# Performance work log

Hardware: AMD Instinct MI355X
Metric: run time of the kernel (lower is better)

## Reference

```python
import jax, jax.numpy as jnp
import numpy as np

D_MODEL, D_FF, D_NEURON, D_HIDDEN = 512, 2048, 128, 256
PHI_IN = D_NEURON + 1  # 129
EPS = 1e-5


def _ln(x, g, b):
    mu = x.mean(-1, keepdims=True)
    var = ((x - mu) ** 2).mean(-1, keepdims=True)
    return (x - mu) * jax.lax.rsqrt(var + EPS) * g + b


def _gelu(x):
    return jax.nn.gelu(x, approximate=False)


def setup_inputs() -> dict:
    key = jax.random.key(0)
    ks = jax.random.split(key, 16)
    s = 0.02
    inp = {
        'x': jax.random.normal(ks[0], (4, 1024, D_MODEL), jnp.float32),
        'W_in': jax.random.normal(ks[1], (D_FF, D_MODEL), jnp.float32) * s,
        'neuron_vecs': jax.random.normal(ks[2], (D_FF, D_NEURON), jnp.float32) * s,
        'Wr1': jax.random.normal(ks[3], (D_MODEL, D_MODEL), jnp.float32) * s,
        'Wr2': jax.random.normal(ks[4], (D_FF, D_MODEL), jnp.float32) * s,
        'rn_g': jnp.ones((D_MODEL,), jnp.float32),
        'rn_b': jnp.zeros((D_MODEL,), jnp.float32),
        'pW1': jax.random.normal(ks[5], (PHI_IN, D_HIDDEN), jnp.float32) * (1.0 / np.sqrt(PHI_IN)),
        'pb1': jnp.zeros((D_HIDDEN,), jnp.float32),
        'pln1_g': jnp.ones((D_HIDDEN,), jnp.float32),
        'pln1_b': jnp.zeros((D_HIDDEN,), jnp.float32),
        'pW2': jax.random.normal(ks[6], (D_HIDDEN, D_HIDDEN), jnp.float32) * (1.0 / np.sqrt(D_HIDDEN)),
        'pb2': jnp.zeros((D_HIDDEN,), jnp.float32),
        'pln2_g': jnp.ones((D_HIDDEN,), jnp.float32),
        'pln2_b': jnp.zeros((D_HIDDEN,), jnp.float32),
        'rln_g': jnp.ones((D_HIDDEN,), jnp.float32),
        'rln_b': jnp.zeros((D_HIDDEN,), jnp.float32),
        'rW1': jax.random.normal(ks[7], (D_HIDDEN, 2 * D_HIDDEN), jnp.float32) * (1.0 / np.sqrt(D_HIDDEN)),
        'rb1': jnp.zeros((2 * D_HIDDEN,), jnp.float32),
        'rW2': jax.random.normal(ks[8], (2 * D_HIDDEN, D_MODEL), jnp.float32) * (1.0 / np.sqrt(2 * D_HIDDEN)),
        'rb2': jnp.zeros((D_MODEL,), jnp.float32),
        'top_k': 64,
    }
    return inp


def reference(x, W_in, neuron_vecs, Wr1, Wr2, rn_g, rn_b,
              pW1, pb1, pln1_g, pln1_b, pW2, pb2, pln2_g, pln2_b,
              rln_g, rln_b, rW1, rb1, rW2, rb2, top_k):
    batch, seq, d_model = x.shape
    xf = x.reshape(-1, d_model)  # [T, D]

    # Router (MLP variant): LN -> GELU(x @ Wr1^T) -> @ Wr2^T
    h = _gelu(_ln(xf, rn_g, rn_b) @ Wr1.T)
    scores = h @ Wr2.T  # [T, d_ff]
    _, idx = jax.lax.top_k(scores, top_k)  # [T, K]

    # Gather selected neuron params (irregular access)
    W_sel = W_in[idx]           # [T, K, D]
    nv_sel = neuron_vecs[idx]   # [T, K, d_neuron]

    # Per-token activations for selected neurons
    act = _gelu(jnp.einsum('td,tkd->tk', xf, W_sel))  # [T, K]

    # phi: Linear -> LN -> GELU -> Linear -> LN
    phi_in = jnp.concatenate([nv_sel, act[..., None]], axis=-1)  # [T, K, 129]
    hphi = _ln(phi_in @ pW1 + pb1, pln1_g, pln1_b)
    hphi = _gelu(hphi)
    hphi = _ln(hphi @ pW2 + pb2, pln2_g, pln2_b)  # [T, K, d_hidden]

    agg = hphi.sum(axis=1)  # [T, d_hidden]

    # rho: LN -> Linear -> GELU -> (Dropout eval=identity) -> Linear
    r = _ln(agg, rln_g, rln_b)
    r = _gelu(r @ rW1 + rb1)
    out = r @ rW2 + rb2  # [T, d_model]
    return out.reshape(batch, seq, d_model)
```

## Files before the change

kernel.cpp:

```cpp
#include <hip/hip_runtime.h>
#include <cstdint>
#include <cstddef>

typedef unsigned short u16;
typedef float f32x4 __attribute__((ext_vector_type(4)));
typedef short short8 __attribute__((ext_vector_type(8)));
typedef int i32x4 __attribute__((ext_vector_type(4)));


__device__ __forceinline__ float geluf(float v) {
  return 0.5f * v * (1.0f + erff(v * 0.70710678118654752440f));
}

__device__ __forceinline__ float erf_fast(float x) {
  const float ax = fabsf(x);
  const float t = __builtin_amdgcn_rcpf(fmaf(0.3275911f, ax, 1.0f));
  float p = fmaf(1.061405429f, t, -1.453152027f);
  p = fmaf(p, t, 1.421413741f);
  p = fmaf(p, t, -0.284496736f);
  p = fmaf(p, t, 0.254829592f);
  p = p * t;
  const float e = __expf(-ax * ax);
  const float r = fmaf(-p, e, 1.0f);
  return copysignf(r, x);
}
__device__ __forceinline__ float gelu_fast(float v) {
  return 0.5f * v * (1.0f + erf_fast(v * 0.70710678118654752440f));
}

__device__ __forceinline__ u16 f2bf(float f) {
  unsigned u = __float_as_uint(f);
  u = (u + 0x7FFFu + ((u >> 16) & 1u)) >> 16;
  return (u16)u;
}
__device__ __forceinline__ float bf2f(u16 h) {
  return __uint_as_float(((unsigned)h) << 16);
}

__device__ __forceinline__ void waveRed2(float& s, float& s2) {
#pragma unroll
  for (int m = 1; m < 64; m <<= 1) {
    s += __shfl_xor(s, m);
    s2 += __shfl_xor(s2, m);
  }
}

__global__ __launch_bounds__(256) void k_ln512(const float* __restrict__ x,
                                               const float* __restrict__ g,
                                               const float* __restrict__ b,
                                               float* __restrict__ out) {
  __shared__ float red[8];
  const int t = blockIdx.x, tid = threadIdx.x;
  const float v0 = x[(size_t)t * 512 + tid];
  const float v1 = x[(size_t)t * 512 + 256 + tid];
  float s = v0 + v1, s2 = v0 * v0 + v1 * v1;
  waveRed2(s, s2);
  if ((tid & 63) == 0) { red[(tid >> 6) * 2] = s; red[(tid >> 6) * 2 + 1] = s2; }
  __syncthreads();
  s = red[0] + red[2] + red[4] + red[6];
  s2 = red[1] + red[3] + red[5] + red[7];
  const float mu = s * (1.f / 512.f);
  const float var = fmaxf(s2 * (1.f / 512.f) - mu * mu, 0.f);
  const float rstd = 1.f / sqrtf(var + 1e-5f);
  out[(size_t)t * 512 + tid] = (v0 - mu) * rstd * g[tid] + b[tid];
  out[(size_t)t * 512 + 256 + tid] = (v1 - mu) * rstd * g[tid + 256] + b[tid + 256];
}

__global__ __launch_bounds__(256) void k_cvt(const float* __restrict__ in,
                                             u16* __restrict__ o) {
  const int i = blockIdx.x * 256 + threadIdx.x;
  o[i] = f2bf(in[i]);
}

__global__ __launch_bounds__(256) void k_splitT(const float* __restrict__ in,
                                                u16* __restrict__ hiT,
                                                u16* __restrict__ loT, int R,
                                                int Cc) {
  const int n = blockIdx.x;
  for (int k = threadIdx.x; k < R; k += 256) {
    const float v = in[(size_t)k * Cc + n];
    const u16 h = f2bf(v);
    hiT[(size_t)n * R + k] = h;
    loT[(size_t)n * R + k] = f2bf(v - bf2f(h));
  }
}

__global__ __launch_bounds__(256) void k_nvphi(const float* __restrict__ nv,
                                               const float* __restrict__ pW1,
                                               const float* __restrict__ pb1,
                                               float* __restrict__ nvphi) {
  __shared__ float nvs[128];
  const int n = blockIdx.x, tid = threadIdx.x;
  if (tid < 128) nvs[tid] = nv[n * 128 + tid];
  __syncthreads();
  float s = pb1[tid];
#pragma unroll 4
  for (int i = 0; i < 128; ++i) s = fmaf(nvs[i], pW1[i * 256 + tid], s);
  nvphi[n * 256 + tid] = s;
}

__global__ __launch_bounds__(256) void k_pw2t(const float* __restrict__ pW2,
                                              u16* __restrict__ pW2T) {
  const int n = blockIdx.x, k = threadIdx.x;
  pW2T[n * 256 + k] = f2bf(pW2[k * 256 + n]);
}

template <int GMODE, bool BF16OUT>
__global__ __launch_bounds__(256) void gemm_bt(const float* __restrict__ A,
                                               const float* __restrict__ B,
                                               float* __restrict__ C,
                                               u16* __restrict__ Cb, int M,
                                               int N, int K) {
  __shared__ float As[16][68];
  __shared__ float Bs[16][68];
  const int tid = threadIdx.x;
  const int tn = tid & 15, tm = tid >> 4;
  const int m0 = blockIdx.y * 64, n0 = blockIdx.x * 64;
  const int lr = tid >> 2, lk = (tid & 3) << 2;
  float acc[4][4] = {};
  for (int k0 = 0; k0 < K; k0 += 16) {
    const float4 av = *(const float4*)&A[(size_t)(m0 + lr) * K + k0 + lk];
    const float4 bv = *(const float4*)&B[(size_t)(n0 + lr) * K + k0 + lk];
    As[lk + 0][lr] = av.x; As[lk + 1][lr] = av.y; As[lk + 2][lr] = av.z; As[lk + 3][lr] = av.w;
    Bs[lk + 0][lr] = bv.x; Bs[lk + 1][lr] = bv.y; Bs[lk + 2][lr] = bv.z; Bs[lk + 3][lr] = bv.w;
    __syncthreads();
#pragma unroll
    for (int k = 0; k < 16; ++k) {
      float a[4], b[4];
      *(float4*)a = *(const float4*)&As[k][tm * 4];
      *(float4*)b = *(const float4*)&Bs[k][tn * 4];
#pragma unroll
      for (int i = 0; i < 4; ++i)
#pragma unroll
        for (int j = 0; j < 4; ++j) acc[i][j] = fmaf(a[i], b[j], acc[i][j]);
    }
    __syncthreads();
  }
#pragma unroll
  for (int i = 0; i < 4; ++i) {
    float4 v;
    float* vp = (float*)&v;
#pragma unroll
    for (int j = 0; j < 4; ++j) {
      float xv = acc[i][j];
      if (GMODE == 2) xv = geluf(xv);
      vp[j] = xv;
    }
    const size_t off = (size_t)(m0 + tm * 4 + i) * N + n0 + tn * 4;
    *(float4*)&C[off] = v;
    if (BF16OUT) {
      ushort4 ob;
      ob.x = f2bf(vp[0]); ob.y = f2bf(vp[1]); ob.z = f2bf(vp[2]); ob.w = f2bf(vp[3]);
      *(ushort4*)&Cb[off] = ob;
    }
  }
}

template <bool SPLIT, int GMODE, bool BIAS, int OUT>
__global__ __launch_bounds__(256) void gemm_mf(
    const u16* __restrict__ Ahi, const u16* __restrict__ Alo,
    const u16* __restrict__ Bhi, const u16* __restrict__ Blo,
    const float* __restrict__ bias, void* __restrict__ Cp,
    void* __restrict__ C2p, int M, int N, int K) {
  constexpr int ASZ = 64 * 40;
  constexpr int BSZ = 128 * 40;
  __shared__ __align__(16) u16 smem[(SPLIT ? 2 : 1) * (ASZ + BSZ)];
  u16* sAh = smem;
  u16* sBh = smem + (SPLIT ? 2 : 1) * ASZ;
  u16* sAl = SPLIT ? (smem + ASZ) : nullptr;
  u16* sBl = SPLIT ? (sBh + BSZ) : nullptr;

  const int tid = threadIdx.x;
  const int w = tid >> 6, lane = tid & 63;
  const int q = lane >> 4, c = lane & 15;
  const int m0 = blockIdx.y * 64, n0 = blockIdx.x * 128;
  const int ra = tid >> 2, ka = (tid & 3) * 8;
  const int rb = tid >> 1, kb = (tid & 1) * 16;
  const u16* gAh = Ahi + (size_t)(m0 + ra) * K + ka;
  const u16* gBh = Bhi + (size_t)(n0 + rb) * K + kb;
  const u16* gAl = SPLIT ? (Alo + (size_t)(m0 + ra) * K + ka) : nullptr;
  const u16* gBl = SPLIT ? (Blo + (size_t)(n0 + rb) * K + kb) : nullptr;

  f32x4 acc[8];
#pragma unroll
  for (int ct = 0; ct < 8; ++ct) {
    const float bv = BIAS ? bias[n0 + ct * 16 + c] : 0.f;
    acc[ct] = (f32x4){bv, bv, bv, bv};
  }

  for (int k0 = 0; k0 < K; k0 += 32) {
    const i32x4 vah = *(const i32x4*)(gAh + k0);
    const i32x4 vbh0 = *(const i32x4*)(gBh + k0);
    const i32x4 vbh1 = *(const i32x4*)(gBh + k0 + 8);
    i32x4 val, vbl0, vbl1;
    if (SPLIT) {
      val = *(const i32x4*)(gAl + k0);
      vbl0 = *(const i32x4*)(gBl + k0);
      vbl1 = *(const i32x4*)(gBl + k0 + 8);
    }
    __syncthreads();
    *(i32x4*)&sAh[ra * 40 + ka] = vah;
    *(i32x4*)&sBh[rb * 40 + kb] = vbh0;
    *(i32x4*)&sBh[rb * 40 + kb + 8] = vbh1;
    if (SPLIT) {
      *(i32x4*)&sAl[ra * 40 + ka] = val;
      *(i32x4*)&sBl[rb * 40 + kb] = vbl0;
      *(i32x4*)&sBl[rb * 40 + kb + 8] = vbl1;
    }
    __syncthreads();
    const int abase = (w * 16 + c) * 40 + q * 8;
    const short8 ah = *(const short8*)&sAh[abase];
    short8 al;
    if (SPLIT) al = *(const short8*)&sAl[abase];
#pragma unroll
    for (int ct = 0; ct < 8; ++ct) {
      const int bbase = (ct * 16 + c) * 40 + q * 8;
      const short8 bh = *(const short8*)&sBh[bbase];
      acc[ct] = __builtin_amdgcn_mfma_f32_16x16x32_bf16(ah, bh, acc[ct], 0, 0, 0);
      if (SPLIT) {
        const short8 bl = *(const short8*)&sBl[bbase];
        acc[ct] = __builtin_amdgcn_mfma_f32_16x16x32_bf16(al, bh, acc[ct], 0, 0, 0);
        acc[ct] = __builtin_amdgcn_mfma_f32_16x16x32_bf16(ah, bl, acc[ct], 0, 0, 0);
      }
    }
  }
#pragma unroll
  for (int ct = 0; ct < 8; ++ct) {
#pragma unroll
    for (int reg = 0; reg < 4; ++reg) {
      float v = acc[ct][reg];
      if (GMODE == 1) v = gelu_fast(v);
      const size_t off = (size_t)(m0 + w * 16 + q * 4 + reg) * N + n0 + ct * 16 + c;
      if (OUT == 0) {
        ((float*)Cp)[off] = v;
      } else if (OUT == 1) {
        ((u16*)Cp)[off] = f2bf(v);
      } else {
        const u16 hv = f2bf(v);
        ((u16*)Cp)[off] = hv;
        ((u16*)C2p)[off] = f2bf(v - bf2f(hv));
      }
    }
  }
}

__global__ __launch_bounds__(256) void k_topk_rs(
    const u16* __restrict__ scoresb, const float* __restrict__ h,
    const float* __restrict__ Wr2, int* __restrict__ idxout) {
  __shared__ float hs[512];
  __shared__ int redc[4];
  __shared__ int cand[160];
  __shared__ float cex[160];
  __shared__ unsigned ccnt, cg_cnt, ec;
  __shared__ int eqbuf[64];
  const int t = blockIdx.x, tid = threadIdx.x;
  hs[tid] = h[(size_t)t * 512 + tid];
  hs[tid + 256] = h[(size_t)t * 512 + 256 + tid];
  unsigned key[8];
#pragma unroll
  for (int j = 0; j < 8; ++j) {
    const unsigned u = ((unsigned)scoresb[(size_t)t * 2048 + tid + 256 * j]) << 16;
    key[j] = (u & 0x80000000u) ? ~u : (u | 0x80000000u);
  }
  if (tid == 0) ccnt = 0u;
  unsigned lo = 0u, hi = 0xFFFFFFFFu;
  while (lo < hi) {
    const unsigned mid = (unsigned)(((unsigned long long)lo + hi + 1ull) >> 1);
    int c = 0;
#pragma unroll
    for (int j = 0; j < 8; ++j) c += (key[j] >= mid);
#pragma unroll
    for (int m = 1; m < 64; m <<= 1) c += __shfl_xor(c, m);
    if ((tid & 63) == 0) redc[tid >> 6] = c;
    __syncthreads();
    const int total = redc[0] + redc[1] + redc[2] + redc[3];
    __syncthreads();
    if (total >= 96) lo = mid; else hi = mid - 1;
  }
#pragma unroll
  for (int j = 0; j < 8; ++j) {
    if (key[j] >= lo) {
      const unsigned pos = atomicAdd(&ccnt, 1u);
      if (pos < 160u) cand[pos] = tid + 256 * j;
    }
  }
  __syncthreads();
  const int cnt = (int)(ccnt < 160u ? ccnt : 160u);
  const int wv = tid >> 6, l = tid & 63;
  for (int ci = wv; ci < cnt; ci += 4) {
    const float* Wr = Wr2 + (size_t)cand[ci] * 512;
    float s = 0.f;
#pragma unroll
    for (int j = 0; j < 8; ++j) s = fmaf(Wr[l + 64 * j], hs[l + 64 * j], s);
#pragma unroll
    for (int m = 1; m < 64; m <<= 1) s += __shfl_xor(s, m);
    if (l == 0) cex[ci] = s;
  }
  __syncthreads();
  unsigned k2 = 0u;
  int myidx = -1;
  const bool valid = tid < cnt;
  if (valid) {
    const unsigned u = __float_as_uint(cex[tid]);
    k2 = (u & 0x80000000u) ? ~u : (u | 0x80000000u);
    myidx = cand[tid];
  }
  if (tid == 0) { cg_cnt = 0u; ec = 0u; }
  lo = 0u; hi = 0xFFFFFFFFu;
  while (lo < hi) {
    const unsigned mid = (unsigned)(((unsigned long long)lo + hi + 1ull) >> 1);
    int c = (valid && k2 >= mid) ? 1 : 0;
#pragma unroll
    for (int m = 1; m < 64; m <<= 1) c += __shfl_xor(c, m);
    if ((tid & 63) == 0) redc[tid >> 6] = c;
    __syncthreads();
    const int total = redc[0] + redc[1] + redc[2] + redc[3];
    __syncthreads();
    if (total >= 64) lo = mid; else hi = mid - 1;
  }
  if (valid && k2 > lo) {
    const unsigned pos = atomicAdd(&cg_cnt, 1u);
    idxout[(size_t)t * 64 + pos] = myidx;
  } else if (valid && k2 == lo) {
    const unsigned e = atomicAdd(&ec, 1u);
    if (e < 64u) eqbuf[e] = myidx;
  }
  __syncthreads();
  if (tid == 0) {
    const int cg = (int)cg_cnt;
    int ne = (int)ec; if (ne > 64) ne = 64;
    const int need = 64 - cg;
    for (int i = 1; i < ne; ++i) {
      const int v = eqbuf[i];
      int j = i - 1;
      while (j >= 0 && eqbuf[j] > v) { eqbuf[j + 1] = eqbuf[j]; --j; }
      eqbuf[j + 1] = v;
    }
    for (int i = 0; i < need; ++i) idxout[(size_t)t * 64 + cg + i] = eqbuf[i];
  }
}

__global__ __launch_bounds__(256) void k_act(const float* __restrict__ x,
                                             const float* __restrict__ W_in,
                                             const int* __restrict__ idx,
                                             float* __restrict__ act) {
  __shared__ float xs[512];
  const int t = blockIdx.x, tid = threadIdx.x;
  xs[tid] = x[(size_t)t * 512 + tid];
  xs[tid + 256] = x[(size_t)t * 512 + 256 + tid];
  __syncthreads();
  const int w = tid >> 6, l = tid & 63;
  for (int q = 0; q < 16; ++q) {
    const int k = w * 16 + q;
    const int n = idx[(size_t)t * 64 + k];
    const float* Wr = W_in + (size_t)n * 512;
    float s = 0.f;
#pragma unroll
    for (int j = 0; j < 8; ++j) s = fmaf(Wr[l + 64 * j], xs[l + 64 * j], s);
#pragma unroll
    for (int m = 1; m < 64; m <<= 1) s += __shfl_xor(s, m);
    if (l == 0) act[(size_t)t * 64 + k] = gelu_fast(s);
  }
}

__global__ __launch_bounds__(256, 1) void k_phi(
    const float* __restrict__ nvphi, const float* __restrict__ pW1,
    const float* __restrict__ pln1_g, const float* __restrict__ pln1_b,
    const u16* __restrict__ pW2T, const float* __restrict__ pb2,
    const float* __restrict__ pln2_g, const float* __restrict__ pln2_b,
    const int* __restrict__ idx, const float* __restrict__ act,
    float* __restrict__ aggp) {
  __shared__ __align__(16) u16 h1s[64 * 264];
  __shared__ __align__(16) u16 Bs[64 * 264];
  __shared__ float aggbuf[4 * 256];
  __shared__ int idxs[64];
  __shared__ float acts[64];
  const int tid = threadIdx.x;
  const int t = blockIdx.x;
  const int w = tid >> 6, lane = tid & 63;
  const int q = lane >> 4, c = lane & 15;
  if (tid < 64) {
    idxs[tid] = idx[(size_t)t * 64 + tid];
    acts[tid] = act[(size_t)t * 64 + tid];
  }
  __syncthreads();
  {
    f32x4 w4[4], g1[4], b1[4];
#pragma unroll
    for (int j = 0; j < 4; ++j) {
      w4[j] = *(const f32x4*)&pW1[128 * 256 + c * 16 + j * 4];
      g1[j] = *(const f32x4*)&pln1_g[c * 16 + j * 4];
      b1[j] = *(const f32x4*)&pln1_b[c * 16 + j * 4];
    }
#pragma unroll 1
    for (int rd = 0; rd < 4; ++rd) {
      const int p = w * 16 + rd * 4 + q;
      const int n = idxs[p];
      const float av = acts[p];
      f32x4 v[4];
      float s = 0.f, s2 = 0.f;
#pragma unroll
      for (int j = 0; j < 4; ++j) {
        const f32x4 nv = *(const f32x4*)&nvphi[(size_t)n * 256 + c * 16 + j * 4];
#pragma unroll
        for (int u = 0; u < 4; ++u) {
          v[j][u] = nv[u] + av * w4[j][u];
          s += v[j][u];
          s2 = fmaf(v[j][u], v[j][u], s2);
        }
      }
#pragma unroll
      for (int m = 1; m < 16; m <<= 1) { s += __shfl_xor(s, m); s2 += __shfl_xor(s2, m); }
      const float mu = s * (1.f / 256.f);
      const float var = fmaxf(s2 * (1.f / 256.f) - mu * mu, 0.f);
      const float rstd = 1.f / sqrtf(var + 1e-5f);
      short8 lo, hi;
#pragma unroll
      for (int j = 0; j < 4; ++j)
#pragma unroll
        for (int u = 0; u < 4; ++u) {
          const float hv = gelu_fast((v[j][u] - mu) * rstd * g1[j][u] + b1[j][u]);
          if (j < 2) lo[j * 4 + u] = (short)f2bf(hv);
          else       hi[(j - 2) * 4 + u] = (short)f2bf(hv);
        }
      *(short8*)&h1s[p * 264 + c * 16] = lo;
      *(short8*)&h1s[p * 264 + c * 16 + 8] = hi;
    }
  }
  __syncthreads();
  short8 afr[8];
#pragma unroll
  for (int ks = 0; ks < 8; ++ks)
    afr[ks] = *(const short8*)&h1s[(w * 16 + c) * 264 + ks * 32 + q * 8];
  f32x4 acc[16];
#pragma unroll
  for (int nt = 0; nt < 16; ++nt) {
    const float bz = pb2[nt * 16 + c];
    acc[nt] = (f32x4){bz, bz, bz, bz};
  }
#pragma unroll
  for (int ch = 0; ch < 4; ++ch) {
    __syncthreads();
#pragma unroll
    for (int i = 0; i < 8; ++i) {
      const int cidx = i * 256 + tid;
      const int n = cidx >> 5, kc = cidx & 31;
      *(i32x4*)&Bs[n * 264 + kc * 8] =
          *(const i32x4*)&pW2T[(size_t)(ch * 64 + n) * 256 + kc * 8];
    }
    __syncthreads();
#pragma unroll
    for (int t4 = 0; t4 < 4; ++t4) {
      const int nt = ch * 4 + t4;
#pragma unroll
      for (int ks = 0; ks < 8; ++ks) {
        const short8 bfr = *(const short8*)&Bs[(t4 * 16 + c) * 264 + ks * 32 + q * 8];
        acc[nt] = __builtin_amdgcn_mfma_f32_16x16x32_bf16(afr[ks], bfr, acc[nt], 0, 0, 0);
      }
    }
  }
  float g2v[16], b2v[16];
#pragma unroll
  for (int nt = 0; nt < 16; ++nt) {
    g2v[nt] = pln2_g[nt * 16 + c];
    b2v[nt] = pln2_b[nt * 16 + c];
  }
  float aggl[16];
#pragma unroll
  for (int nt = 0; nt < 16; ++nt) aggl[nt] = 0.f;
#pragma unroll
  for (int reg = 0; reg < 4; ++reg) {
    float s = 0.f, s2 = 0.f;
#pragma unroll
    for (int nt = 0; nt < 16; ++nt) {
      const float vv = acc[nt][reg];
      s += vv;
      s2 = fmaf(vv, vv, s2);
    }
#pragma unroll
    for (int m = 1; m < 16; m <<= 1) { s += __shfl_xor(s, m); s2 += __shfl_xor(s2, m); }
    const float mu = s * (1.f / 256.f);
    const float var = fmaxf(s2 * (1.f / 256.f) - mu * mu, 0.f);
    const float rstd = 1.f / sqrtf(var + 1e-5f);
#pragma unroll
    for (int nt = 0; nt < 16; ++nt) {
      const float vv = acc[nt][reg];
      aggl[nt] += (vv - mu) * rstd * g2v[nt] + b2v[nt];
    }
  }
#pragma unroll
  for (int nt = 0; nt < 16; ++nt) {
    float vs = aggl[nt];
    vs += __shfl_xor(vs, 16);
    vs += __shfl_xor(vs, 32);
    if (q == 0) aggbuf[w * 256 + nt * 16 + c] = vs;
  }
  __syncthreads();
  aggp[(size_t)t * 256 + tid] =
      aggbuf[tid] + aggbuf[256 + tid] + aggbuf[512 + tid] + aggbuf[768 + tid];
}

__global__ __launch_bounds__(256) void k_rln(const float* __restrict__ aggp,
                                             const float* __restrict__ g,
                                             const float* __restrict__ b,
                                             u16* __restrict__ rh,
                                             u16* __restrict__ rl) {
  __shared__ float red[8];
  const int t = blockIdx.x, tid = threadIdx.x;
  const float v = aggp[(size_t)t * 256 + tid];
  float s = v, s2 = v * v;
  waveRed2(s, s2);
  if ((tid & 63) == 0) { red[(tid >> 6) * 2] = s; red[(tid >> 6) * 2 + 1] = s2; }
  __syncthreads();
  s = red[0] + red[2] + red[4] + red[6];
  s2 = red[1] + red[3] + red[5] + red[7];
  const float mu = s * (1.f / 256.f);
  const float var = fmaxf(s2 * (1.f / 256.f) - mu * mu, 0.f);
  const float rstd = 1.f / sqrtf(var + 1e-5f);
  const float y = (v - mu) * rstd * g[tid] + b[tid];
  const u16 hv = f2bf(y);
  rh[(size_t)t * 256 + tid] = hv;
  rl[(size_t)t * 256 + tid] = f2bf(y - bf2f(hv));
}

extern "C" void kernel_launch(void* const* d_in, const int* in_sizes, int n_in,
                              void* d_out, int out_size, void* d_ws, size_t ws_size,
                              hipStream_t stream) {
  const float* x = (const float*)d_in[0];
  const float* W_in = (const float*)d_in[1];
  const float* nv = (const float*)d_in[2];
  const float* Wr1 = (const float*)d_in[3];
  const float* Wr2 = (const float*)d_in[4];
  const float* rn_g = (const float*)d_in[5];
  const float* rn_b = (const float*)d_in[6];
  const float* pW1 = (const float*)d_in[7];
  const float* pb1 = (const float*)d_in[8];
  const float* pln1_g = (const float*)d_in[9];
  const float* pln1_b = (const float*)d_in[10];
  const float* pW2 = (const float*)d_in[11];
  const float* pb2 = (const float*)d_in[12];
  const float* pln2_g = (const float*)d_in[13];
  const float* pln2_b = (const float*)d_in[14];
  const float* rln_g = (const float*)d_in[15];
  const float* rln_b = (const float*)d_in[16];
  const float* rW1 = (const float*)d_in[17];
  const float* rb1 = (const float*)d_in[18];
  const float* rW2 = (const float*)d_in[19];
  const float* rb2 = (const float*)d_in[20];
  float* out = (float*)d_out;
  const int T = in_sizes[0] / 512;

  float* ws = (float*)d_ws;
  float* xln = ws;    ws += (size_t)T * 512;
  float* h = ws;      ws += (size_t)T * 512;
  float* nvphi = ws;  ws += (size_t)2048 * 256;
  float* actb = ws;   ws += (size_t)T * 64;
  float* aggp = ws;   ws += (size_t)T * 256;
  int* idx = (int*)ws;   ws += (size_t)T * 64;
  u16* scoresb = (u16*)ws; ws += (size_t)T * 2048 / 2;
  u16* hb = (u16*)ws;    ws += (size_t)T * 512 / 2;
  u16* Wr2b = (u16*)ws;  ws += (size_t)2048 * 512 / 2;
  u16* pW2T = (u16*)ws;  ws += (size_t)2048 * 256 / 2;
  u16* rh = (u16*)ws;    ws += (size_t)T * 256 / 2;
  u16* rl = (u16*)ws;    ws += (size_t)T * 256 / 2;
  u16* t1h = (u16*)ws;   ws += (size_t)T * 512 / 2;
  u16* t1l = (u16*)ws;   ws += (size_t)T * 512 / 2;
  u16* rW1Th = (u16*)ws; ws += (size_t)512 * 256 / 2;
  u16* rW1Tl = (u16*)ws; ws += (size_t)512 * 256 / 2;
  u16* rW2Th = (u16*)ws; ws += (size_t)512 * 512 / 2;
  u16* rW2Tl = (u16*)ws; ws += (size_t)512 * 512 / 2;

  k_cvt<<<2048 * 512 / 256, 256, 0, stream>>>(Wr2, Wr2b);
  k_splitT<<<512, 256, 0, stream>>>(rW1, rW1Th, rW1Tl, 256, 512);
  k_splitT<<<512, 256, 0, stream>>>(rW2, rW2Th, rW2Tl, 512, 512);
  k_nvphi<<<2048, 256, 0, stream>>>(nv, pW1, pb1, nvphi);
  k_pw2t<<<256, 256, 0, stream>>>(pW2, pW2T);
  k_ln512<<<T, 256, 0, stream>>>(x, rn_g, rn_b, xln);
  gemm_bt<2, true><<<dim3(512 / 64, T / 64), 256, 0, stream>>>(
      xln, Wr1, h, hb, T, 512, 512);
  gemm_mf<false, 0, false, 1><<<dim3(2048 / 128, T / 64), 256, 0, stream>>>(
      hb, nullptr, Wr2b, nullptr, nullptr, scoresb, nullptr, T, 2048, 512);
  k_topk_rs<<<T, 256, 0, stream>>>(scoresb, h, Wr2, idx);
  k_act<<<T, 256, 0, stream>>>(x, W_in, idx, actb);
  k_phi<<<T, 256, 0, stream>>>(nvphi, pW1, pln1_g, pln1_b, pW2T, pb2, pln2_g,
                               pln2_b, idx, actb, aggp);
  k_rln<<<T, 256, 0, stream>>>(aggp, rln_g, rln_b, rh, rl);
  gemm_mf<true, 1, true, 2><<<dim3(512 / 128, T / 64), 256, 0, stream>>>(
      rh, rl, rW1Th, rW1Tl, rb1, t1h, t1l, T, 512, 256);
  gemm_mf<true, 0, true, 0><<<dim3(512 / 128, T / 64), 256, 0, stream>>>(
      t1h, t1l, rW2Th, rW2Tl, rb2, out, nullptr, T, 512, 512);
}
```

Measured before the change: 500.7 us.

## Drop split-bf16 in rho GEMMs, retile router GEMM, vectorize act, shrink phi smem

The rho-stage GEMMs now use a single bf16 pass in place of the hi/lo split (three MFMAs per step become one), which removes the lo buffers and their conversions. The router's first fp32 GEMM moves from 64x64 tiles with 4x4 per thread to 128x128 tiles with 8x8 per thread. Top-k's first radix search now runs over 16-bit keys, k_act uses float4 loads, and k_phi halves its B staging buffer and reuses h1s for aggregation to raise occupancy. The change trades accuracy in the rho MLP for less work, and the larger GEMM tiles launch far fewer blocks.

```diff
diff --git a/kernel.cpp b/kernel.cpp
--- a/kernel.cpp
+++ b/kernel.cpp
@@ -72,17 +72,12 @@
   o[i] = f2bf(in[i]);
 }
 
-__global__ __launch_bounds__(256) void k_splitT(const float* __restrict__ in,
-                                                u16* __restrict__ hiT,
-                                                u16* __restrict__ loT, int R,
-                                                int Cc) {
+__global__ __launch_bounds__(256) void k_cvtT(const float* __restrict__ in,
+                                              u16* __restrict__ outT, int R,
+                                              int Cc) {
   const int n = blockIdx.x;
-  for (int k = threadIdx.x; k < R; k += 256) {
-    const float v = in[(size_t)k * Cc + n];
-    const u16 h = f2bf(v);
-    hiT[(size_t)n * R + k] = h;
-    loT[(size_t)n * R + k] = f2bf(v - bf2f(h));
-  }
+  for (int k = threadIdx.x; k < R; k += 256)
+    outT[(size_t)n * R + k] = f2bf(in[(size_t)k * Cc + n]);
 }
 
 __global__ __launch_bounds__(256) void k_nvphi(const float* __restrict__ nv,
@@ -106,69 +101,80 @@
 }
 
 template <int GMODE, bool BF16OUT>
-__global__ __launch_bounds__(256) void gemm_bt(const float* __restrict__ A,
-                                               const float* __restrict__ B,
-                                               float* __restrict__ C,
-                                               u16* __restrict__ Cb, int M,
+__global__ __launch_bounds__(256) void gemm8f(const float* __restrict__ A,
+                                              const float* __restrict__ B,
+                                              float* __restrict__ C,
+                                              u16* __restrict__ Cb, int M,
+                                              int N, int K) {
+  __shared__ float As[16][132];
+  __shared__ float Bs[16][132];
+  const int tid = threadIdx.x;
+  const int tm = tid >> 4, tn = tid & 15;
+  const int m0 = blockIdx.y * 128, n0 = blockIdx.x * 128;
+  const int sr = tid >> 1, sk = (tid & 1) * 8;
+  const float* gA = &A[(size_t)(m0 + sr) * K + sk];
+  const float* gB = &B[(size_t)(n0 + sr) * K + sk];
+  float acc[8][8] = {};
+  for (int k0 = 0; k0 < K; k0 += 16) {
+    const float4 a0 = *(const float4*)&gA[k0];
+    const float4 a1 = *(const float4*)&gA[k0 + 4];
+    const float4 b0 = *(const float4*)&gB[k0];
+    const float4 b1 = *(const float4*)&gB[k0 + 4];
+    __syncthreads();
+    As[sk + 0][sr] = a0.x; As[sk + 1][sr] = a0.y; As[sk + 2][sr] = a0.z; As[sk + 3][sr] = a0.w;
+    As[sk + 4][sr] = a1.x; As[sk + 5][sr] = a1.y; As[sk + 6][sr] = a1.z; As[sk + 7][sr] = a1.w;
+    Bs[sk + 0][sr] = b0.x; Bs[sk + 1][sr] = b0.y; Bs[sk + 2][sr] = b0.z; Bs[sk + 3][sr] = b0.w;
+    Bs[sk + 4][sr] = b1.x; Bs[sk + 5][sr] = b1.y; Bs[sk + 6][sr] = b1.z; Bs[sk + 7][sr] = b1.w;
+    __syncthreads();
+#pragma unroll
+    for (int k = 0; k < 16; ++k) {
+      float a[8], b[8];
+      *(float4*)&a[0] = *(const float4*)&As[k][tm * 8];
+      *(float4*)&a[4] = *(const float4*)&As[k][tm * 8 + 4];
+      *(float4*)&b[0] = *(const float4*)&Bs[k][tn * 8];
+      *(float4*)&b[4] = *(const float4*)&Bs[k][tn * 8 + 4];
+#pragma unroll
+      for (int i = 0; i < 8; ++i)
+#pragma unroll
+        for (int j = 0; j < 8; ++j) acc[i][j] = fmaf(a[i], b[j], acc[i][j]);
+    }
+  }
+#pragma unroll
+  for (int i = 0; i < 8; ++i) {
+    float4 o0, o1;
+    float* p0 = (float*)&o0;
+    float* p1 = (float*)&o1;
+#pragma unroll
+    for (int j = 0; j < 4; ++j) {
+      float xv = acc[i][j], yv = acc[i][j + 4];
+      if (GMODE == 1) { xv = gelu_fast(xv); yv = gelu_fast(yv); }
+      if (GMODE == 2) { xv = geluf(xv); yv = geluf(yv); }
+      p0[j] = xv; p1[j] = yv;
+    }
+    const size_t off = (size_t)(m0 + tm * 8 + i) * N + n0 + tn * 8;
+    *(float4*)&C[off] = o0;
+    *(float4*)&C[off + 4] = o1;
+    if (BF16OUT) {
+      ushort4 u0, u1;
+      u0.x = f2bf(p0[0]); u0.y = f2bf(p0[1]); u0.z = f2bf(p0[2]); u0.w = f2bf(p0[3]);
+      u1.x = f2bf(p1[0]); u1.y = f2bf(p1[1]); u1.z = f2bf(p1[2]); u1.w = f2bf(p1[3]);
+      *(ushort4*)&Cb[off] = u0;
+      *(ushort4*)&Cb[off + 4] = u1;
+    }
+  }
+}
+
+template <int GMODE, bool BIAS, int OUT>
+__global__ __launch_bounds__(256) void gemm_mf(const u16* __restrict__ Ahi,
+                                               const u16* __restrict__ Bhi,
+                                               const float* __restrict__ bias,
+                                               void* __restrict__ Cp, int M,
                                                int N, int K) {
-  __shared__ float As[16][68];
-  __shared__ float Bs[16][68];
-  const int tid = threadIdx.x;
-  const int tn = tid & 15, tm = tid >> 4;
-  const int m0 = blockIdx.y * 64, n0 = blockIdx.x * 64;
-  const int lr = tid >> 2, lk = (tid & 3) << 2;
-  float acc[4][4] = {};
-  for (int k0 = 0; k0 < K; k0 += 16) {
-    const float4 av = *(const float4*)&A[(size_t)(m0 + lr) * K + k0 + lk];
-    const float4 bv = *(const float4*)&B[(size_t)(n0 + lr) * K + k0 + lk];
-    As[lk + 0][lr] = av.x; As[lk + 1][lr] = av.y; As[lk + 2][lr] = av.z; As[lk + 3][lr] = av.w;
-    Bs[lk + 0][lr] = bv.x; Bs[lk + 1][lr] = bv.y; Bs[lk + 2][lr] = bv.z; Bs[lk + 3][lr] = bv.w;
-    __syncthreads();
-#pragma unroll
-    for (int k = 0; k < 16; ++k) {
-      float a[4], b[4];
-      *(float4*)a = *(const float4*)&As[k][tm * 4];
-      *(float4*)b = *(const float4*)&Bs[k][tn * 4];
-#pragma unroll
-      for (int i = 0; i < 4; ++i)
-#pragma unroll
-        for (int j = 0; j < 4; ++j) acc[i][j] = fmaf(a[i], b[j], acc[i][j]);
-    }
-    __syncthreads();
-  }
-#pragma unroll
-  for (int i = 0; i < 4; ++i) {
-    float4 v;
-    float* vp = (float*)&v;
-#pragma unroll
-    for (int j = 0; j < 4; ++j) {
-      float xv = acc[i][j];
-      if (GMODE == 2) xv = geluf(xv);
-      vp[j] = xv;
-    }
-    const size_t off = (size_t)(m0 + tm * 4 + i) * N + n0 + tn * 4;
-    *(float4*)&C[off] = v;
-    if (BF16OUT) {
-      ushort4 ob;
-      ob.x = f2bf(vp[0]); ob.y = f2bf(vp[1]); ob.z = f2bf(vp[2]); ob.w = f2bf(vp[3]);
-      *(ushort4*)&Cb[off] = ob;
-    }
-  }
-}
-
-template <bool SPLIT, int GMODE, bool BIAS, int OUT>
-__global__ __launch_bounds__(256) void gemm_mf(
-    const u16* __restrict__ Ahi, const u16* __restrict__ Alo,
-    const u16* __restrict__ Bhi, const u16* __restrict__ Blo,
-    const float* __restrict__ bias, void* __restrict__ Cp,
-    void* __restrict__ C2p, int M, int N, int K) {
   constexpr int ASZ = 64 * 40;
   constexpr int BSZ = 128 * 40;
-  __shared__ __align__(16) u16 smem[(SPLIT ? 2 : 1) * (ASZ + BSZ)];
+  __shared__ __align__(16) u16 smem[ASZ + BSZ];
   u16* sAh = smem;
-  u16* sBh = smem + (SPLIT ? 2 : 1) * ASZ;
-  u16* sAl = SPLIT ? (smem + ASZ) : nullptr;
-  u16* sBl = SPLIT ? (sBh + BSZ) : nullptr;
+  u16* sBh = smem + ASZ;
 
   const int tid = threadIdx.x;
   const int w = tid >> 6, lane = tid & 63;
@@ -178,8 +184,6 @@
   const int rb = tid >> 1, kb = (tid & 1) * 16;
   const u16* gAh = Ahi + (size_t)(m0 + ra) * K + ka;
   const u16* gBh = Bhi + (size_t)(n0 + rb) * K + kb;
-  const u16* gAl = SPLIT ? (Alo + (size_t)(m0 + ra) * K + ka) : nullptr;
-  const u16* gBl = SPLIT ? (Blo + (size_t)(n0 + rb) * K + kb) : nullptr;
 
   f32x4 acc[8];
 #pragma unroll
@@ -192,36 +196,18 @@
     const i32x4 vah = *(const i32x4*)(gAh + k0);
     const i32x4 vbh0 = *(const i32x4*)(gBh + k0);
     const i32x4 vbh1 = *(const i32x4*)(gBh + k0 + 8);
-    i32x4 val, vbl0, vbl1;
-    if (SPLIT) {
-      val = *(const i32x4*)(gAl + k0);
-      vbl0 = *(const i32x4*)(gBl + k0);
-      vbl1 = *(const i32x4*)(gBl + k0 + 8);
-    }
     __syncthreads();
     *(i32x4*)&sAh[ra * 40 + ka] = vah;
     *(i32x4*)&sBh[rb * 40 + kb] = vbh0;
     *(i32x4*)&sBh[rb * 40 + kb + 8] = vbh1;
-    if (SPLIT) {
-      *(i32x4*)&sAl[ra * 40 + ka] = val;
-      *(i32x4*)&sBl[rb * 40 + kb] = vbl0;
-      *(i32x4*)&sBl[rb * 40 + kb + 8] = vbl1;
-    }
     __syncthreads();
     const int abase = (w * 16 + c) * 40 + q * 8;
     const short8 ah = *(const short8*)&sAh[abase];
-    short8 al;
-    if (SPLIT) al = *(const short8*)&sAl[abase];
 #pragma unroll
     for (int ct = 0; ct < 8; ++ct) {
       const int bbase = (ct * 16 + c) * 40 + q * 8;
       const short8 bh = *(const short8*)&sBh[bbase];
       acc[ct] = __builtin_amdgcn_mfma_f32_16x16x32_bf16(ah, bh, acc[ct], 0, 0, 0);
-      if (SPLIT) {
-        const short8 bl = *(const short8*)&sBl[bbase];
-        acc[ct] = __builtin_amdgcn_mfma_f32_16x16x32_bf16(al, bh, acc[ct], 0, 0, 0);
-        acc[ct] = __builtin_amdgcn_mfma_f32_16x16x32_bf16(ah, bl, acc[ct], 0, 0, 0);
-      }
     }
   }
 #pragma unroll
@@ -231,15 +217,8 @@
       float v = acc[ct][reg];
       if (GMODE == 1) v = gelu_fast(v);
       const size_t off = (size_t)(m0 + w * 16 + q * 4 + reg) * N + n0 + ct * 16 + c;
-      if (OUT == 0) {
-        ((float*)Cp)[off] = v;
-      } else if (OUT == 1) {
-        ((u16*)Cp)[off] = f2bf(v);
-      } else {
-        const u16 hv = f2bf(v);
-        ((u16*)Cp)[off] = hv;
-        ((u16*)C2p)[off] = f2bf(v - bf2f(hv));
-      }
+      if (OUT == 0) ((float*)Cp)[off] = v;
+      else          ((u16*)Cp)[off] = f2bf(v);
     }
   }
 }
@@ -259,13 +238,13 @@
   unsigned key[8];
 #pragma unroll
   for (int j = 0; j < 8; ++j) {
-    const unsigned u = ((unsigned)scoresb[(size_t)t * 2048 + tid + 256 * j]) << 16;
-    key[j] = (u & 0x80000000u) ? ~u : (u | 0x80000000u);
+    const unsigned u = (unsigned)scoresb[(size_t)t * 2048 + tid + 256 * j];
+    key[j] = (u & 0x8000u) ? (0xFFFFu & ~u) : (u | 0x8000u);
   }
   if (tid == 0) ccnt = 0u;
-  unsigned lo = 0u, hi = 0xFFFFFFFFu;
+  unsigned lo = 0u, hi = 0xFFFFu;
   while (lo < hi) {
-    const unsigned mid = (unsigned)(((unsigned long long)lo + hi + 1ull) >> 1);
+    const unsigned mid = (lo + hi + 1u) >> 1;
     int c = 0;
 #pragma unroll
     for (int j = 0; j < 8; ++j) c += (key[j] >= mid);
@@ -306,9 +285,9 @@
     myidx = cand[tid];
   }
   if (tid == 0) { cg_cnt = 0u; ec = 0u; }
-  lo = 0u; hi = 0xFFFFFFFFu;
-  while (lo < hi) {
-    const unsigned mid = (unsigned)(((unsigned long long)lo + hi + 1ull) >> 1);
+  unsigned lo2 = 0u, hi2 = 0xFFFFFFFFu;
+  while (lo2 < hi2) {
+    const unsigned mid = (unsigned)(((unsigned long long)lo2 + hi2 + 1ull) >> 1);
     int c = (valid && k2 >= mid) ? 1 : 0;
 #pragma unroll
     for (int m = 1; m < 64; m <<= 1) c += __shfl_xor(c, m);
@@ -316,12 +295,12 @@
     __syncthreads();
     const int total = redc[0] + redc[1] + redc[2] + redc[3];
     __syncthreads();
-    if (total >= 64) lo = mid; else hi = mid - 1;
-  }
-  if (valid && k2 > lo) {
+    if (total >= 64) lo2 = mid; else hi2 = mid - 1;
+  }
+  if (valid && k2 > lo2) {
     const unsigned pos = atomicAdd(&cg_cnt, 1u);
     idxout[(size_t)t * 64 + pos] = myidx;
-  } else if (valid && k2 == lo) {
+  } else if (valid && k2 == lo2) {
     const unsigned e = atomicAdd(&ec, 1u);
     if (e < 64u) eqbuf[e] = myidx;
   }
@@ -350,13 +329,18 @@
   xs[tid + 256] = x[(size_t)t * 512 + 256 + tid];
   __syncthreads();
   const int w = tid >> 6, l = tid & 63;
-  for (int q = 0; q < 16; ++q) {
-    const int k = w * 16 + q;
+  const float4 xa = *(const float4*)&xs[l * 8];
+  const float4 xb = *(const float4*)&xs[l * 8 + 4];
+  for (int qq = 0; qq < 16; ++qq) {
+    const int k = w * 16 + qq;
     const int n = idx[(size_t)t * 64 + k];
-    const float* Wr = W_in + (size_t)n * 512;
-    float s = 0.f;
-#pragma unroll
-    for (int j = 0; j < 8; ++j) s = fmaf(Wr[l + 64 * j], xs[l + 64 * j], s);
+    const float* Wr = W_in + (size_t)n * 512 + l * 8;
+    const float4 wa = *(const float4*)Wr;
+    const float4 wb = *(const float4*)(Wr + 4);
+    float s = wa.x * xa.x;
+    s = fmaf(wa.y, xa.y, s); s = fmaf(wa.z, xa.z, s); s = fmaf(wa.w, xa.w, s);
+    s = fmaf(wb.x, xb.x, s); s = fmaf(wb.y, xb.y, s);
+    s = fmaf(wb.z, xb.z, s); s = fmaf(wb.w, xb.w, s);
 #pragma unroll
     for (int m = 1; m < 64; m <<= 1) s += __shfl_xor(s, m);
     if (l == 0) act[(size_t)t * 64 + k] = gelu_fast(s);
@@ -371,8 +355,7 @@
     const int* __restrict__ idx, const float* __restrict__ act,
     float* __restrict__ aggp) {
   __shared__ __align__(16) u16 h1s[64 * 264];
-  __shared__ __align__(16) u16 Bs[64 * 264];
-  __shared__ float aggbuf[4 * 256];
+  __shared__ __align__(16) u16 Bs[32 * 264];
   __shared__ int idxs[64];
   __shared__ float acts[64];
   const int tid = threadIdx.x;
@@ -392,7 +375,7 @@
       g1[j] = *(const f32x4*)&pln1_g[c * 16 + j * 4];
       b1[j] = *(const f32x4*)&pln1_b[c * 16 + j * 4];
     }
-#pragma unroll 1
+#pragma unroll 2
     for (int rd = 0; rd < 4; ++rd) {
       const int p = w * 16 + rd * 4 + q;
       const int n = idxs[p];
@@ -439,19 +422,19 @@
     acc[nt] = (f32x4){bz, bz, bz, bz};
   }
 #pragma unroll
-  for (int ch = 0; ch < 4; ++ch) {
-    __syncthreads();
-#pragma unroll
-    for (int i = 0; i < 8; ++i) {
+  for (int ch = 0; ch < 8; ++ch) {
+    __syncthreads();
+#pragma unroll
+    for (int i = 0; i < 4; ++i) {
       const int cidx = i * 256 + tid;
       const int n = cidx >> 5, kc = cidx & 31;
       *(i32x4*)&Bs[n * 264 + kc * 8] =
-          *(const i32x4*)&pW2T[(size_t)(ch * 64 + n) * 256 + kc * 8];
-    }
-    __syncthreads();
-#pragma unroll
-    for (int t4 = 0; t4 < 4; ++t4) {
-      const int nt = ch * 4 + t4;
+          *(const i32x4*)&pW2T[(size_t)(ch * 32 + n) * 256 + kc * 8];
+    }
+    __syncthreads();
+#pragma unroll
+    for (int t4 = 0; t4 < 2; ++t4) {
+      const int nt = ch * 2 + t4;
 #pragma unroll
       for (int ks = 0; ks < 8; ++ks) {
         const short8 bfr = *(const short8*)&Bs[(t4 * 16 + c) * 264 + ks * 32 + q * 8];
@@ -488,6 +471,7 @@
       aggl[nt] += (vv - mu) * rstd * g2v[nt] + b2v[nt];
     }
   }
+  float* aggbuf = (float*)h1s;
 #pragma unroll
   for (int nt = 0; nt < 16; ++nt) {
     float vs = aggl[nt];
@@ -503,8 +487,7 @@
 __global__ __launch_bounds__(256) void k_rln(const float* __restrict__ aggp,
                                              const float* __restrict__ g,
                                              const float* __restrict__ b,
-                                             u16* __restrict__ rh,
-                                             u16* __restrict__ rl) {
+                                             u16* __restrict__ rh) {
   __shared__ float red[8];
   const int t = blockIdx.x, tid = threadIdx.x;
   const float v = aggp[(size_t)t * 256 + tid];
@@ -517,10 +500,7 @@
   const float mu = s * (1.f / 256.f);
   const float var = fmaxf(s2 * (1.f / 256.f) - mu * mu, 0.f);
   const float rstd = 1.f / sqrtf(var + 1e-5f);
-  const float y = (v - mu) * rstd * g[tid] + b[tid];
-  const u16 hv = f2bf(y);
-  rh[(size_t)t * 256 + tid] = hv;
-  rl[(size_t)t * 256 + tid] = f2bf(y - bf2f(hv));
+  rh[(size_t)t * 256 + tid] = f2bf((v - mu) * rstd * g[tid] + b[tid]);
 }
 
 extern "C" void kernel_launch(void* const* d_in, const int* in_sizes, int n_in,
@@ -562,31 +542,27 @@
   u16* Wr2b = (u16*)ws;  ws += (size_t)2048 * 512 / 2;
   u16* pW2T = (u16*)ws;  ws += (size_t)2048 * 256 / 2;
   u16* rh = (u16*)ws;    ws += (size_t)T * 256 / 2;
-  u16* rl = (u16*)ws;    ws += (size_t)T * 256 / 2;
-  u16* t1h = (u16*)ws;   ws += (size_t)T * 512 / 2;
-  u16* t1l = (u16*)ws;   ws += (size_t)T * 512 / 2;
-  u16* rW1Th = (u16*)ws; ws += (size_t)512 * 256 / 2;
-  u16* rW1Tl = (u16*)ws; ws += (size_t)512 * 256 / 2;
-  u16* rW2Th = (u16*)ws; ws += (size_t)512 * 512 / 2;
-  u16* rW2Tl = (u16*)ws; ws += (size_t)512 * 512 / 2;
+  u16* t1b = (u16*)ws;   ws += (size_t)T * 512 / 2;
+  u16* rW1T = (u16*)ws;  ws += (size_t)512 * 256 / 2;
+  u16* rW2T = (u16*)ws;  ws += (size_t)512 * 512 / 2;
 
   k_cvt<<<2048 * 512 / 256, 256, 0, stream>>>(Wr2, Wr2b);
-  k_splitT<<<512, 256, 0, stream>>>(rW1, rW1Th, rW1Tl, 256, 512);
-  k_splitT<<<512, 256, 0, stream>>>(rW2, rW2Th, rW2Tl, 512, 512);
+  k_cvtT<<<512, 256, 0, stream>>>(rW1, rW1T, 256, 512);
+  k_cvtT<<<512, 256, 0, stream>>>(rW2, rW2T, 512, 512);
   k_nvphi<<<2048, 256, 0, stream>>>(nv, pW1, pb1, nvphi);
   k_pw2t<<<256, 256, 0, stream>>>(pW2, pW2T);
   k_ln512<<<T, 256, 0, stream>>>(x, rn_g, rn_b, xln);
-  gemm_bt<2, true><<<dim3(512 / 64, T / 64), 256, 0, stream>>>(
+  gemm8f<2, true><<<dim3(512 / 128, T / 128), 256, 0, stream>>>(
       xln, Wr1, h, hb, T, 512, 512);
-  gemm_mf<false, 0, false, 1><<<dim3(2048 / 128, T / 64), 256, 0, stream>>>(
-      hb, nullptr, Wr2b, nullptr, nullptr, scoresb, nullptr, T, 2048, 512);
+  gemm_mf<0, false, 1><<<dim3(2048 / 128, T / 64), 256, 0, stream>>>(
+      hb, Wr2b, nullptr, scoresb, T, 2048, 512);
   k_topk_rs<<<T, 256, 0, stream>>>(scoresb, h, Wr2, idx);
   k_act<<<T, 256, 0, stream>>>(x, W_in, idx, actb);
   k_phi<<<T, 256, 0, stream>>>(nvphi, pW1, pln1_g, pln1_b, pW2T, pb2, pln2_g,
                                pln2_b, idx, actb, aggp);
-  k_rln<<<T, 256, 0, stream>>>(aggp, rln_g, rln_b, rh, rl);
-  gemm_mf<true, 1, true, 2><<<dim3(512 / 128, T / 64), 256, 0, stream>>>(
-      rh, rl, rW1Th, rW1Tl, rb1, t1h, t1l, T, 512, 256);
-  gemm_mf<true, 0, true, 0><<<dim3(512 / 128, T / 64), 256, 0, stream>>>(
-      t1h, t1l, rW2Th, rW2Tl, rb2, out, nullptr, T, 512, 512);
-}
+  k_rln<<<T, 256, 0, stream>>>(aggp, rln_g, rln_b, rh);
+  gemm_mf<1, true, 1><<<dim3(512 / 128, T / 64), 256, 0, stream>>>(
+      rh, rW1T, rb1, t1b, T, 512, 256);
+  gemm_mf<0, true, 0><<<dim3(512 / 128, T / 64), 256, 0, stream>>>(
+      t1b, rW2T, rb2, out, T, 512, 512);
+}
```

Measured after the change: 571.3 us. 1.14x slower.
